# Optimization experiments

Measured on AMD Instinct MI355X. Metric: run time of the kernel, lower is better.

Reference implementation:

```python
import jax, jax.numpy as jnp
import numpy as np

TINY = 1e-15
EPS = 1e-6  # float32 eps from the torch module
C = 1.0
S = 1.0 / np.sqrt(C)
SQRTC = np.sqrt(C)


def _sinhc(z):
    # stable sinh(z)/z with small-argument Taylor branch
    y = jnp.sinh(z) / jnp.maximum(z, EPS)
    y0 = 1.0 + z * z / 6.0
    return jnp.where(jnp.abs(z) < EPS, y0, y)


def _beta(x):
    denom = jnp.sqrt(1.0 + C * jnp.sum(x * x, axis=-1, keepdims=True))
    return 1.0 / jnp.maximum(denom, TINY)


def _log0(y):
    s = jnp.linalg.norm(y, axis=-1, keepdims=True)
    coef = jnp.arcsinh(s / S) / jnp.maximum(s / S, EPS)
    return coef * y


def _exp0(v):
    r = jnp.linalg.norm(v, axis=-1, keepdims=True)
    coef = jnp.sinh(r / S) / jnp.maximum(r / S, EPS)
    return coef * v


def _proj_tan0(v, max_norm=20.0):
    r = jnp.maximum(jnp.linalg.norm(v, axis=-1, keepdims=True), EPS)
    return jnp.minimum(max_norm / r, 1.0) * v


def _pt_0_to_y(y, v):
    b = _beta(y)
    coef = C * b / (1.0 + b)
    dot = jnp.sum(y * v, axis=-1, keepdims=True)
    return v + coef * dot * y


def _gyro_add(x, y):
    b_x = _beta(x)
    b_y = _beta(y)
    s2 = S * S
    xy = jnp.sum(x * y, axis=-1, keepdims=True)
    coef = b_x / (1.0 + b_x) * (xy / s2) + (1.0 - b_y) / b_y
    return x + y + coef * x


def _exp_map(x, v):
    s2 = S * S
    x_norm2 = jnp.sum(x * x, axis=-1, keepdims=True)
    v_norm2 = jnp.sum(v * v, axis=-1, keepdims=True)
    dot_x_v = jnp.sum(x * v, axis=-1, keepdims=True)
    g_pvv = jnp.maximum(v_norm2 - dot_x_v * dot_x_v / (s2 + x_norm2), TINY)
    r_g = jnp.sqrt(g_pvv)
    b_x = _beta(x)
    coef1 = b_x / (1.0 + b_x)
    coef2 = -(C * b_x ** 3) / jnp.maximum(1.0 + b_x, TINY) ** 2
    dpi_v = coef1 * v + coef2 * dot_x_v * x
    lambda_x = (1.0 + b_x) / jnp.maximum(b_x, TINY)
    z_arg = jnp.clip(SQRTC * r_g, -20.0, 20.0)
    w = lambda_x * _sinhc(z_arg) * dpi_v
    return _gyro_add(x, w)


def setup_inputs() -> dict:
    key = jax.random.key(0)
    k1, k2, k3 = jax.random.split(key, 3)
    N, D_IN, D_OUT = 16384, 2048, 2048
    x = jax.random.normal(k1, (N, D_IN), dtype=jnp.float32)
    # weight scaled ~1/sqrt(d_in) so tangent norms stay in a sane hyperbolic range
    W = jax.random.normal(k2, (D_OUT, D_IN), dtype=jnp.float32) * (1.0 / np.sqrt(D_IN))
    b = jax.random.normal(k3, (D_OUT,), dtype=jnp.float32) * 0.01
    return {"x": x, "W": W, "b": b}


def reference(x, W, b):
    # PV fully-connected layer: log map -> linear -> exp map -> transported bias
    v = _log0(x)                 # [N, d_in] tangent at origin
    u = v @ W.T                  # [N, d_out]
    u = _proj_tan0(u)            # tangent norm clamp (max_norm=20)
    y = _exp0(u)                 # [N, d_out] PV point
    bt = _pt_0_to_y(y, b)        # parallel transport bias tangent 0 -> y
    out = _exp_map(y, bt)        # geodesic step (includes gyro_add)
    return out
```

## Files before the change

kernel.cpp:

```cpp
#include <hip/hip_runtime.h>
#include <stdint.h>

typedef __bf16 bf16_t;
typedef __bf16 bf16x8 __attribute__((ext_vector_type(8)));
typedef float floatx4 __attribute__((ext_vector_type(4)));

#define N_ROWS 16384
#define D_IN   2048
#define D_OUT  2048
#define EPSF   1e-6f
#define TINYF  1e-15f

#define BM 256
#define BN 256
#define BK 64
#define NT 96

__device__ __forceinline__ void load_lds16(const void* g, void* l) {
    __builtin_amdgcn_global_load_lds(
        (const __attribute__((address_space(1))) unsigned int*)(const unsigned int*)g,
        (__attribute__((address_space(3))) unsigned int*)(unsigned int*)l,
        16, 0, 0);
}

__global__ __launch_bounds__(256) void pvfc_wsplit(
    const float* __restrict__ W, bf16_t* __restrict__ Wh, bf16_t* __restrict__ Wl)
{
    const size_t i = ((size_t)blockIdx.x * 256 + threadIdx.x) * 8;
    float4 a = *(const float4*)(W + i);
    float4 c = *(const float4*)(W + i + 4);
    float v[8] = {a.x, a.y, a.z, a.w, c.x, c.y, c.z, c.w};
    bf16x8 hv, lv;
#pragma unroll
    for (int j = 0; j < 8; ++j) {
        const bf16_t h = (bf16_t)v[j];
        hv[j] = h;
        lv[j] = (bf16_t)(v[j] - (float)h);
    }
    *(bf16x8*)(Wh + i) = hv;
    *(bf16x8*)(Wl + i) = lv;
}

__global__ __launch_bounds__(256) void pvfc_prologue(
    const float* __restrict__ x, bf16_t* __restrict__ Ap)
{
    __shared__ float red[4];
    const int row = blockIdx.x, tid = threadIdx.x;
    const int lane = tid & 63, wave = tid >> 6;

    const float* xr = x + (size_t)row * D_IN + tid * 8;
    float4 a = *(const float4*)xr;
    float4 c = *(const float4*)(xr + 4);
    float v[8] = {a.x, a.y, a.z, a.w, c.x, c.y, c.z, c.w};

    float s = 0.f;
#pragma unroll
    for (int i = 0; i < 8; ++i) s += v[i] * v[i];
#pragma unroll
    for (int off = 32; off > 0; off >>= 1) s += __shfl_down(s, off, 64);
    if (lane == 0) red[wave] = s;
    __syncthreads();
    const float s2  = red[0] + red[1] + red[2] + red[3];
    const float nrm = sqrtf(s2);
    const float coef = asinhf(nrm) / fmaxf(nrm, EPSF);

    bf16x8 hv, lv;
#pragma unroll
    for (int j = 0; j < 8; ++j) {
        const float vi = coef * v[j];
        const bf16_t h = (bf16_t)vi;
        hv[j] = h;
        lv[j] = (bf16_t)(vi - (float)h);
    }
    bf16_t* ar = Ap + (size_t)row * (2 * D_IN);
    *(bf16x8*)(ar + tid * 8)         = hv;
    *(bf16x8*)(ar + D_IN + tid * 8)  = lv;
}

#define BAR __builtin_amdgcn_s_barrier()
#define WAIT_LGKM0 do { asm volatile("s_waitcnt lgkmcnt(0)" ::: "memory"); \
                        __builtin_amdgcn_sched_barrier(0); } while (0)
#define WAIT_VM2   do { asm volatile("s_waitcnt vmcnt(2)" ::: "memory");   \
                        __builtin_amdgcn_sched_barrier(0); } while (0)

#define LOAD_A(buf, qm)                                                        \
    _Pragma("unroll")                                                          \
    for (int i = 0; i < 4; ++i) {                                              \
        const int rA = wm * 128 + ((qm) * 4 + i) * 16 + m16;                   \
        _Pragma("unroll")                                                      \
        for (int ks = 0; ks < 2; ++ks)                                         \
            af[i][ks] = *(const bf16x8*)&As[buf][rA * BK +                     \
                                                 (((ks * 4 + quad) ^ sw) * 8)];\
    }

#define LOAD_B(buf, qn, bq)                                                    \
    _Pragma("unroll")                                                          \
    for (int j = 0; j < 2; ++j) {                                              \
        const int rB = wn * 64 + ((qn) * 2 + j) * 16 + m16;                    \
        _Pragma("unroll")                                                      \
        for (int ks = 0; ks < 2; ++ks)                                         \
            bq[j][ks] = *(const bf16x8*)&Bs[buf][rB * BK +                     \
                                                 (((ks * 4 + quad) ^ sw) * 8)];\
    }

#define MFMA_Q(qm, qn, bq)                                                     \
    do {                                                                       \
        __builtin_amdgcn_sched_barrier(0);                                     \
        __builtin_amdgcn_s_setprio(1);                                         \
        _Pragma("unroll")                                                      \
        for (int ks = 0; ks < 2; ++ks)                                         \
            _Pragma("unroll")                                                  \
            for (int i = 0; i < 4; ++i)                                        \
                _Pragma("unroll")                                              \
                for (int j = 0; j < 2; ++j)                                    \
                    acc[(qm) * 4 + i][(qn) * 2 + j] =                          \
                        __builtin_amdgcn_mfma_f32_16x16x32_bf16(               \
                            af[i][ks], bq[j][ks],                              \
                            acc[(qm) * 4 + i][(qn) * 2 + j], 0, 0, 0);         \
        __builtin_amdgcn_s_setprio(0);                                         \
        __builtin_amdgcn_sched_barrier(0);                                     \
    } while (0)

__global__ __launch_bounds__(512, 2) void pvfc_gemm(
    const bf16_t* __restrict__ A,
    const bf16_t* __restrict__ Wh, const bf16_t* __restrict__ Wl,
    float* __restrict__ U)
{
    __shared__ __align__(16) bf16_t As[2][BM * BK];
    __shared__ __align__(16) bf16_t Bs[2][BN * BK];

    const int tid  = threadIdx.x;
    const int wave = tid >> 6, lane = tid & 63;
    const int bid  = blockIdx.x;
    const int colBase = (bid & 7) * BN;
    const int rowBase = (bid >> 3) * BM;

    const int wm = wave >> 2, wn = wave & 3;
    const int m16 = lane & 15, quad = lane >> 4;
    const int sw  = m16 & 7;

    const int sRow = tid >> 3;
    const int sCol = ((tid & 7) ^ (sRow & 7)) * 8;
    const int ldsOff = wave * 512;

    floatx4 acc[8][4];
    bf16x8 af[4][2], bq0[2][2], bq1[2][2];
    const floatx4 z = {0.f, 0.f, 0.f, 0.f};
#pragma unroll
    for (int i = 0; i < 8; ++i)
#pragma unroll
        for (int j = 0; j < 4; ++j) acc[i][j] = z;

    auto stageA = [&](int tile, int half, int buf) {
        const int tt  = tile < NT ? tile : NT - 1;
        const int seg = tt >> 5;
        const size_t off = (size_t)((seg == 1) ? D_IN : 0) + (size_t)(tt & 31) * BK;
        const bf16_t* src = A + (size_t)(rowBase + half * 128 + sRow) * (2 * D_IN)
                              + off + sCol;
        bf16_t* dst = &As[buf][half * 128 * BK + ldsOff];
        load_lds16(src, dst);
        load_lds16(src + (size_t)64 * (2 * D_IN), dst + 64 * BK);
    };
    auto stageB = [&](int tile, int half, int buf) {
        const int tt  = tile < NT ? tile : NT - 1;
        const bf16_t* Wp = ((tt >> 5) == 2) ? Wl : Wh;
        const int k0 = (tt & 31) * BK;
        const bf16_t* src = Wp + (size_t)(colBase + half * 128 + sRow) * D_IN
                               + k0 + sCol;
        bf16_t* dst = &Bs[buf][half * 128 * BK + ldsOff];
        load_lds16(src, dst);
        load_lds16(src + (size_t)64 * D_IN, dst + 64 * BK);
    };

    stageA(0, 0, 0); stageA(0, 1, 0); stageB(0, 0, 0); stageB(0, 1, 0);
    stageA(1, 0, 1);
    WAIT_VM2;
    BAR;

#pragma clang loop unroll(disable)
    for (int t = 0; t < NT; t += 2) {
        LOAD_A(0, 0); LOAD_B(0, 0, bq0);
        stageA(t + 1, 1, 1);
        BAR; WAIT_LGKM0; MFMA_Q(0, 0, bq0); BAR;

        LOAD_B(0, 1, bq1);
        stageB(t + 1, 0, 1);
        BAR; WAIT_LGKM0; MFMA_Q(0, 1, bq1); BAR;

        LOAD_A(0, 1);
        stageB(t + 1, 1, 1);
        BAR; WAIT_LGKM0; MFMA_Q(1, 1, bq1); BAR;

        stageA(t + 2, 0, 0);
        WAIT_VM2;
        BAR; MFMA_Q(1, 0, bq0); BAR;

        LOAD_A(1, 0); LOAD_B(1, 0, bq0);
        stageA(t + 2, 1, 0);
        BAR; WAIT_LGKM0; MFMA_Q(0, 0, bq0); BAR;

        LOAD_B(1, 1, bq1);
        stageB(t + 2, 0, 0);
        BAR; WAIT_LGKM0; MFMA_Q(0, 1, bq1); BAR;

        LOAD_A(1, 1);
        stageB(t + 2, 1, 0);
        BAR; WAIT_LGKM0; MFMA_Q(1, 1, bq1); BAR;

        stageA(t + 3, 0, 1);
        WAIT_VM2;
        BAR; MFMA_Q(1, 0, bq0); BAR;
    }

#pragma unroll
    for (int mi = 0; mi < 8; ++mi)
#pragma unroll
        for (int ni = 0; ni < 4; ++ni) {
            const int col = colBase + wn * 64 + ni * 16 + m16;
            float* up = U + (size_t)(rowBase + wm * 128 + mi * 16 + quad * 4) * D_OUT
                          + col;
#pragma unroll
            for (int r = 0; r < 4; ++r)
                up[(size_t)r * D_OUT] = acc[mi][ni][r];
        }
}

__global__ __launch_bounds__(256) void pvfc_epilogue(
    const float* __restrict__ U, const float* __restrict__ bvec,
    float* __restrict__ out)
{
    __shared__ float red[12];
    const int row = blockIdx.x, tid = threadIdx.x;
    const int lane = tid & 63, wave = tid >> 6;

    const float* ur = U + (size_t)row * D_OUT + tid * 8;
    float u[8];
    { float4 a = *(const float4*)ur, c = *(const float4*)(ur + 4);
      u[0]=a.x;u[1]=a.y;u[2]=a.z;u[3]=a.w;u[4]=c.x;u[5]=c.y;u[6]=c.z;u[7]=c.w; }
    float b[8];
    { const float* br = bvec + tid * 8;
      float4 a = *(const float4*)br, c = *(const float4*)(br + 4);
      b[0]=a.x;b[1]=a.y;b[2]=a.z;b[3]=a.w;b[4]=c.x;b[5]=c.y;b[6]=c.z;b[7]=c.w; }

    float su2 = 0.f, sub = 0.f, sbb = 0.f;
#pragma unroll
    for (int i = 0; i < 8; ++i) { su2 += u[i]*u[i]; sub += u[i]*b[i]; sbb += b[i]*b[i]; }
#pragma unroll
    for (int off = 32; off > 0; off >>= 1) {
        su2 += __shfl_down(su2, off, 64);
        sub += __shfl_down(sub, off, 64);
        sbb += __shfl_down(sbb, off, 64);
    }
    if (lane == 0) { red[wave] = su2; red[4 + wave] = sub; red[8 + wave] = sbb; }
    __syncthreads();
    su2 = red[0] + red[1] + red[2] + red[3];
    sub = red[4] + red[5] + red[6] + red[7];
    sbb = red[8] + red[9] + red[10] + red[11];

    const float r0 = sqrtf(su2);
    const float t  = fminf(20.f / fmaxf(r0, EPSF), 1.f);
    const float rp = t * r0;
    const float coef_e = sinhf(rp) / fmaxf(rp, EPSF);
    const float P  = coef_e * t;
    const float yn2 = P * P * su2;
    const float beta = 1.f / fmaxf(sqrtf(1.f + yn2), TINYF);
    const float c  = beta / (1.f + beta);
    const float d  = P * sub;
    const float vn2   = sbb + c * d * d * (2.f + c * yn2);
    const float dotxv = d * (1.f + c * yn2);
    const float g  = fmaxf(vn2 - dotxv * dotxv / (1.f + yn2), TINYF);
    const float rg = sqrtf(g);
    const float coef1 = beta / (1.f + beta);
    const float t1 = fmaxf(1.f + beta, TINYF);
    const float coef2 = -(beta * beta * beta) / (t1 * t1);
    const float lam = (1.f + beta) / fmaxf(beta, TINYF);
    const float z  = fminf(rg, 20.f);
    const float sc = (fabsf(z) < EPSF) ? (1.f + z * z * (1.f / 6.f))
                                       : (sinhf(z) / fmaxf(z, EPSF));
    const float L = lam * sc;
    const float alpha = L * coef1;
    const float gamma = L * (coef1 * c * d + coef2 * dotxv);
    const float wn2 = alpha * alpha * sbb + 2.f * alpha * gamma * d + gamma * gamma * yn2;
    const float bw  = 1.f / fmaxf(sqrtf(1.f + wn2), TINYF);
    const float xy  = alpha * d + gamma * yn2;
    const float coefg = coef1 * xy + (1.f - bw) / bw;
    const float Ascale = P * (1.f + gamma + coefg);

    float* orow = out + (size_t)row * D_OUT + tid * 8;
    float4 o0, o1;
    o0.x = Ascale*u[0] + alpha*b[0]; o0.y = Ascale*u[1] + alpha*b[1];
    o0.z = Ascale*u[2] + alpha*b[2]; o0.w = Ascale*u[3] + alpha*b[3];
    o1.x = Ascale*u[4] + alpha*b[4]; o1.y = Ascale*u[5] + alpha*b[5];
    o1.z = Ascale*u[6] + alpha*b[6]; o1.w = Ascale*u[7] + alpha*b[7];
    *(float4*)orow       = o0;
    *(float4*)(orow + 4) = o1;
}

extern "C" void kernel_launch(void* const* d_in, const int* in_sizes, int n_in,
                              void* d_out, int out_size, void* d_ws, size_t ws_size,
                              hipStream_t stream)
{
    const float* x = (const float*)d_in[0];
    const float* W = (const float*)d_in[1];
    const float* b = (const float*)d_in[2];
    float* out = (float*)d_out;

    bf16_t* Wh = (bf16_t*)d_ws;
    bf16_t* Wl = Wh + (size_t)D_OUT * D_IN;
    char*   rest = (char*)(Wl + (size_t)D_OUT * D_IN);
    const size_t wbytes = (size_t)D_OUT * D_IN * 2 * 2;
    const size_t avail  = (ws_size > wbytes) ? ws_size - wbytes : 0;
    int chunk = (int)((avail / 16384 / 256) * 256);
    if (chunk <= 0) chunk = 256;
    if (chunk > N_ROWS) chunk = N_ROWS;

    bf16_t* Ap = (bf16_t*)rest;
    float*  U  = (float*)(rest + (size_t)chunk * (2 * D_IN) * 2);

    pvfc_wsplit<<<(D_OUT * D_IN) / (256 * 8), 256, 0, stream>>>(W, Wh, Wl);
    for (int r0 = 0; r0 < N_ROWS; r0 += chunk) {
        const int rows = (N_ROWS - r0 < chunk) ? (N_ROWS - r0) : chunk;
        pvfc_prologue<<<rows, 256, 0, stream>>>(x + (size_t)r0 * D_IN, Ap);
        pvfc_gemm<<<(rows / 256) * 8, 512, 0, stream>>>(Ap, Wh, Wl, U);
        pvfc_epilogue<<<rows, 256, 0, stream>>>(U, b, out + (size_t)r0 * D_OUT);
    }
}
```

Baseline: 721.5 us.

## Restructure GEMM main loop into per-tile bodies with fewer barriers, add nontemporal memory ops

Replaces the hand-interleaved GEMM loop, which had many barriers and staged quarter-tile prefetches, with a simpler per-tile body. Each body issues the whole next-tile prefetch up front, computes the current tile using two A-fragment register sets, then waits for all loads and synchronises once. This cuts the number of workgroup barriers and lgkm waits per tile, at the cost of more registers and a full vmcnt(0) wait at the end of each tile. Separately, the x loads in the prologue, the U stores and loads, and the output stores become nontemporal to reduce cache pollution from streaming data.

Result: faster. 635.5 us (-11.9%).

```diff
diff --git a/kernel.cpp b/kernel.cpp
--- a/kernel.cpp
+++ b/kernel.cpp
@@ -4,6 +4,7 @@
 typedef __bf16 bf16_t;
 typedef __bf16 bf16x8 __attribute__((ext_vector_type(8)));
 typedef float floatx4 __attribute__((ext_vector_type(4)));
+typedef float f32x4 __attribute__((ext_vector_type(4)));
 
 #define N_ROWS 16384
 #define D_IN   2048
@@ -27,8 +28,8 @@
     const float* __restrict__ W, bf16_t* __restrict__ Wh, bf16_t* __restrict__ Wl)
 {
     const size_t i = ((size_t)blockIdx.x * 256 + threadIdx.x) * 8;
-    float4 a = *(const float4*)(W + i);
-    float4 c = *(const float4*)(W + i + 4);
+    f32x4 a = *(const f32x4*)(W + i);
+    f32x4 c = *(const f32x4*)(W + i + 4);
     float v[8] = {a.x, a.y, a.z, a.w, c.x, c.y, c.z, c.w};
     bf16x8 hv, lv;
 #pragma unroll
@@ -49,8 +50,8 @@
     const int lane = tid & 63, wave = tid >> 6;
 
     const float* xr = x + (size_t)row * D_IN + tid * 8;
-    float4 a = *(const float4*)xr;
-    float4 c = *(const float4*)(xr + 4);
+    f32x4 a = __builtin_nontemporal_load((const f32x4*)xr);
+    f32x4 c = __builtin_nontemporal_load((const f32x4*)(xr + 4));
     float v[8] = {a.x, a.y, a.z, a.w, c.x, c.y, c.z, c.w};
 
     float s = 0.f;
@@ -78,18 +79,17 @@
 }
 
 #define BAR __builtin_amdgcn_s_barrier()
-#define WAIT_LGKM0 do { asm volatile("s_waitcnt lgkmcnt(0)" ::: "memory"); \
-                        __builtin_amdgcn_sched_barrier(0); } while (0)
-#define WAIT_VM2   do { asm volatile("s_waitcnt vmcnt(2)" ::: "memory");   \
-                        __builtin_amdgcn_sched_barrier(0); } while (0)
-
-#define LOAD_A(buf, qm)                                                        \
+#define SCHED_FENCE __builtin_amdgcn_sched_barrier(0)
+#define WAIT_VM0 do { asm volatile("s_waitcnt vmcnt(0)" ::: "memory"); \
+                      __builtin_amdgcn_sched_barrier(0); } while (0)
+
+#define LOAD_AH(buf, qm, AF)                                                   \
     _Pragma("unroll")                                                          \
     for (int i = 0; i < 4; ++i) {                                              \
         const int rA = wm * 128 + ((qm) * 4 + i) * 16 + m16;                   \
         _Pragma("unroll")                                                      \
         for (int ks = 0; ks < 2; ++ks)                                         \
-            af[i][ks] = *(const bf16x8*)&As[buf][rA * BK +                     \
+            AF[i][ks] = *(const bf16x8*)&As[buf][rA * BK +                     \
                                                  (((ks * 4 + quad) ^ sw) * 8)];\
     }
 
@@ -103,9 +103,8 @@
                                                  (((ks * 4 + quad) ^ sw) * 8)];\
     }
 
-#define MFMA_Q(qm, qn, bq)                                                     \
+#define MFMA_Q(AF, BQ, qm, qn)                                                 \
     do {                                                                       \
-        __builtin_amdgcn_sched_barrier(0);                                     \
         __builtin_amdgcn_s_setprio(1);                                         \
         _Pragma("unroll")                                                      \
         for (int ks = 0; ks < 2; ++ks)                                         \
@@ -115,10 +114,27 @@
                 for (int j = 0; j < 2; ++j)                                    \
                     acc[(qm) * 4 + i][(qn) * 2 + j] =                          \
                         __builtin_amdgcn_mfma_f32_16x16x32_bf16(               \
-                            af[i][ks], bq[j][ks],                              \
+                            AF[i][ks], BQ[j][ks],                              \
                             acc[(qm) * 4 + i][(qn) * 2 + j], 0, 0, 0);         \
         __builtin_amdgcn_s_setprio(0);                                         \
-        __builtin_amdgcn_sched_barrier(0);                                     \
+    } while (0)
+
+#define TILE_BODY(rb, sb, st)                                                  \
+    do {                                                                       \
+        stageA(st, 0, sb); stageA(st, 1, sb);                                  \
+        stageB(st, 0, sb); stageB(st, 1, sb);                                  \
+        SCHED_FENCE;                                                           \
+        LOAD_AH(rb, 0, afA); LOAD_B(rb, 0, bq0); LOAD_B(rb, 1, bq1);           \
+        SCHED_FENCE;                                                           \
+        MFMA_Q(afA, bq0, 0, 0);                                                \
+        SCHED_FENCE;                                                           \
+        LOAD_AH(rb, 1, afB);                                                   \
+        SCHED_FENCE;                                                           \
+        MFMA_Q(afA, bq1, 0, 1);                                                \
+        MFMA_Q(afB, bq1, 1, 1);                                                \
+        MFMA_Q(afB, bq0, 1, 0);                                                \
+        WAIT_VM0;                                                              \
+        BAR;                                                                   \
     } while (0)
 
 __global__ __launch_bounds__(512, 2) void pvfc_gemm(
@@ -144,7 +160,7 @@
     const int ldsOff = wave * 512;
 
     floatx4 acc[8][4];
-    bf16x8 af[4][2], bq0[2][2], bq1[2][2];
+    bf16x8 afA[4][2], afB[4][2], bq0[2][2], bq1[2][2];
     const floatx4 z = {0.f, 0.f, 0.f, 0.f};
 #pragma unroll
     for (int i = 0; i < 8; ++i)
@@ -173,43 +189,13 @@
     };
 
     stageA(0, 0, 0); stageA(0, 1, 0); stageB(0, 0, 0); stageB(0, 1, 0);
-    stageA(1, 0, 1);
-    WAIT_VM2;
+    WAIT_VM0;
     BAR;
 
 #pragma clang loop unroll(disable)
     for (int t = 0; t < NT; t += 2) {
-        LOAD_A(0, 0); LOAD_B(0, 0, bq0);
-        stageA(t + 1, 1, 1);
-        BAR; WAIT_LGKM0; MFMA_Q(0, 0, bq0); BAR;
-
-        LOAD_B(0, 1, bq1);
-        stageB(t + 1, 0, 1);
-        BAR; WAIT_LGKM0; MFMA_Q(0, 1, bq1); BAR;
-
-        LOAD_A(0, 1);
-        stageB(t + 1, 1, 1);
-        BAR; WAIT_LGKM0; MFMA_Q(1, 1, bq1); BAR;
-
-        stageA(t + 2, 0, 0);
-        WAIT_VM2;
-        BAR; MFMA_Q(1, 0, bq0); BAR;
-
-        LOAD_A(1, 0); LOAD_B(1, 0, bq0);
-        stageA(t + 2, 1, 0);
-        BAR; WAIT_LGKM0; MFMA_Q(0, 0, bq0); BAR;
-
-        LOAD_B(1, 1, bq1);
-        stageB(t + 2, 0, 0);
-        BAR; WAIT_LGKM0; MFMA_Q(0, 1, bq1); BAR;
-
-        LOAD_A(1, 1);
-        stageB(t + 2, 1, 0);
-        BAR; WAIT_LGKM0; MFMA_Q(1, 1, bq1); BAR;
-
-        stageA(t + 3, 0, 1);
-        WAIT_VM2;
-        BAR; MFMA_Q(1, 0, bq0); BAR;
+        TILE_BODY(0, 1, t + 1);
+        TILE_BODY(1, 0, t + 2);
     }
 
 #pragma unroll
@@ -221,7 +207,7 @@
                           + col;
 #pragma unroll
             for (int r = 0; r < 4; ++r)
-                up[(size_t)r * D_OUT] = acc[mi][ni][r];
+                __builtin_nontemporal_store(acc[mi][ni][r], up + (size_t)r * D_OUT);
         }
 }
 
@@ -235,11 +221,12 @@
 
     const float* ur = U + (size_t)row * D_OUT + tid * 8;
     float u[8];
-    { float4 a = *(const float4*)ur, c = *(const float4*)(ur + 4);
+    { f32x4 a = __builtin_nontemporal_load((const f32x4*)ur);
+      f32x4 c = __builtin_nontemporal_load((const f32x4*)(ur + 4));
       u[0]=a.x;u[1]=a.y;u[2]=a.z;u[3]=a.w;u[4]=c.x;u[5]=c.y;u[6]=c.z;u[7]=c.w; }
     float b[8];
     { const float* br = bvec + tid * 8;
-      float4 a = *(const float4*)br, c = *(const float4*)(br + 4);
+      f32x4 a = *(const f32x4*)br, c = *(const f32x4*)(br + 4);
       b[0]=a.x;b[1]=a.y;b[2]=a.z;b[3]=a.w;b[4]=c.x;b[5]=c.y;b[6]=c.z;b[7]=c.w; }
 
     float su2 = 0.f, sub = 0.f, sbb = 0.f;
@@ -287,13 +274,13 @@
     const float Ascale = P * (1.f + gamma + coefg);
 
     float* orow = out + (size_t)row * D_OUT + tid * 8;
-    float4 o0, o1;
+    f32x4 o0, o1;
     o0.x = Ascale*u[0] + alpha*b[0]; o0.y = Ascale*u[1] + alpha*b[1];
     o0.z = Ascale*u[2] + alpha*b[2]; o0.w = Ascale*u[3] + alpha*b[3];
     o1.x = Ascale*u[4] + alpha*b[4]; o1.y = Ascale*u[5] + alpha*b[5];
     o1.z = Ascale*u[6] + alpha*b[6]; o1.w = Ascale*u[7] + alpha*b[7];
-    *(float4*)orow       = o0;
-    *(float4*)(orow + 4) = o1;
+    __builtin_nontemporal_store(o0, (f32x4*)orow);
+    __builtin_nontemporal_store(o1, (f32x4*)(orow + 4));
 }
 
 extern "C" void kernel_launch(void* const* d_in, const int* in_sizes, int n_in,
@@ -321,7 +308,7 @@
     for (int r0 = 0; r0 < N_ROWS; r0 += chunk) {
         const int rows = (N_ROWS - r0 < chunk) ? (N_ROWS - r0) : chunk;
         pvfc_prologue<<<rows, 256, 0, stream>>>(x + (size_t)r0 * D_IN, Ap);
-        pvfc_gemm<<<(rows / 256) * 8, 512, 0, stream>>>(Ap, Wh, Wl, U);
+        pvfc_gemm<<<dim3(D_OUT / BN * (rows / BM)), 512, 0, stream>>>(Ap, Wh, Wl, U);
         pvfc_epilogue<<<rows, 256, 0, stream>>>(U, b, out + (size_t)r0 * D_OUT);
     }
 }
```
